# Kernel tuning notes

Measured on AMD Instinct MI355X. Metric: run time of the kernel, lower is better.

The kernel has to match this reference:

```python
import jax, jax.numpy as jnp
import numpy as np

BATCH, SEQ, CH, ORDER = 4, 8192, 512, 64


def setup_inputs() -> dict:
    key = jax.random.key(0)
    k1, k2, k3 = jax.random.split(key, 3)
    x = jax.random.normal(k1, (BATCH, SEQ, CH), dtype=jnp.float32)
    # RTF parameters: small init so the denominator polynomial 1 + sum a_i z^-i
    # stays well-conditioned (stable transfer function), as in the FSSM init.
    A = 0.01 * jax.random.normal(k2, (CH, ORDER), dtype=jnp.float32)
    B = 0.01 * jax.random.normal(k3, (CH, ORDER), dtype=jnp.float32)
    h0 = jnp.zeros((1,), dtype=jnp.float32)
    return {"x": x, "A": A, "B": B, "h0": h0}


def _rtf_kernel(A, B, L):
    # Evaluate H(z) = b(z)/a(z) at the L roots of unity, then irfft -> impulse response.
    C = A.shape[0]
    a = jnp.concatenate([jnp.ones((C, 1), A.dtype), A], axis=-1)  # (C, N+1), leading coeff 1
    a_f = jnp.fft.rfft(a, n=L, axis=-1)                           # (C, L//2+1)
    b_f = jnp.fft.rfft(B, n=L, axis=-1)
    return jnp.fft.irfft(b_f / a_f, n=L, axis=-1)                 # (C, L)


def reference(x, A, B, h0):
    Bt, L, C = x.shape
    K = _rtf_kernel(A, B, L)                                      # (C, L)
    n_fft = 2 * L                                                 # causal (linear) convolution
    x_f = jnp.fft.rfft(x, n=n_fft, axis=1)                        # (B, n_fft//2+1, C)
    k_f = jnp.fft.rfft(K, n=n_fft, axis=-1).T[None]               # (1, n_fft//2+1, C)
    h1 = jnp.fft.irfft(x_f * k_f, n=n_fft, axis=1)[:, :L]         # (B, L, C)
    y1 = h1 + h0 * x
    return jax.nn.gelu(y1)
```

## Files before the change

### kernel.cpp

```cpp
#include <hip/hip_runtime.h>
#include <stdint.h>

#define NBATCH 4
#define LSEQ   8192
#define CH     512
#define ORDER  64
#define KTAP   256
#define NW     9

typedef _Float16 half8 __attribute__((ext_vector_type(8)));
typedef __fp16   fp16x2 __attribute__((ext_vector_type(2)));
typedef float    f32x4 __attribute__((ext_vector_type(4)));

#define AFRAG_HALFS  ((size_t)CH * NW * 64 * 8)
#define WS_NEED      (AFRAG_HALFS * 2)

#define XROWB 1584
#define SMEMB (16 * XROWB)
#define PAIRS 392
#define TPB   4

__device__ __forceinline__ uint32_t pkrtz(float lo, float hi) {
    fp16x2 v = __builtin_amdgcn_cvt_pkrtz(lo, hi);
    return __builtin_bit_cast(uint32_t, v);
}

__global__ __launch_bounds__(256) void rtf_afrag(const float* __restrict__ A,
                                                 const float* __restrict__ B,
                                                 const float* __restrict__ h0,
                                                 _Float16* __restrict__ afr) {
    __shared__ float Ksh[4][KTAP];
    const int wv = threadIdx.x >> 6, lane = threadIdx.x & 63;
    const int c  = blockIdx.x * 4 + wv;
    const float a  = A[c * ORDER + lane];
    const float bc = B[c * ORDER + lane];
    const float h0v = h0[0];
    float s = 0.0f;
    for (int t = 0; t < KTAP; ++t) {
        const float s1 = __shfl(s, 0);
        const float bt = (t < ORDER) ? __shfl(bc, t) : 0.0f;
        const float y  = bt + s1;
        float su = __shfl_down(s, 1);
        if (lane == ORDER - 1) su = 0.0f;
        s = su - a * y;
        if (lane == 0) Ksh[wv][t] = (t == 0) ? (y + h0v) : y;
    }
    __syncthreads();
    const int i = lane & 15, g = lane >> 4;
    for (int w = 0; w < NW; ++w) {
        half8 hv;
#pragma unroll
        for (int e = 0; e < 8; ++e) {
            const int t = 32 * w + 15 + i - 8 * g - e;
            hv[e] = (_Float16)((t >= 0 && t < KTAP) ? Ksh[wv][t] : 0.0f);
        }
        *reinterpret_cast<half8*>(afr + ((size_t)(c * NW + w) * 64 + lane) * 8) = hv;
    }
}

__global__ __launch_bounds__(256, 2) void fir_pipe(const float* __restrict__ x,
                                                   const _Float16* __restrict__ afr,
                                                   float* __restrict__ out) {
    __shared__ __align__(16) char  xs[SMEMB];
    __shared__ float lout[16][260];
    const int gid     = blockIdx.x;
    const int logical = (gid & 7) * 64 + (gid >> 3);
    const int chgrp   = logical >> 4;
    const int bb      = (logical >> 2) & 3;
    const int qt      = logical & 3;
    const int nbase   = qt * (TPB * 512);
    const int c0      = chgrp * 16;

    const int q  = threadIdx.x & 3;
    const int pr = threadIdx.x >> 2;
    const float* xsrc = x + (size_t)bb * LSEQ * CH + c0 + q * 4;

    f32x4 L0[7], L1[7];

#define LOAD_TILE(N0K)                                                        \
    {                                                                         \
        _Pragma("unroll")                                                     \
        for (int i = 0; i < 7; ++i) {                                         \
            const int p = pr + 64 * i;                                        \
            f32x4 z = {0.f, 0.f, 0.f, 0.f};                                   \
            L0[i] = z; L1[i] = z;                                             \
            if (p < PAIRS) {                                                  \
                const int r0 = (N0K) - 271 + 2 * p;                           \
                if ((unsigned)r0 < LSEQ)                                      \
                    L0[i] = *reinterpret_cast<const f32x4*>(xsrc + (size_t)r0 * CH); \
                if ((unsigned)(r0 + 1) < LSEQ)                                \
                    L1[i] = *reinterpret_cast<const f32x4*>(xsrc + (size_t)(r0 + 1) * CH); \
            }                                                                 \
        }                                                                     \
    }

#define WRITE_XS()                                                            \
    {                                                                         \
        _Pragma("unroll")                                                     \
        for (int i = 0; i < 7; ++i) {                                         \
            const int p = pr + 64 * i;                                        \
            if (p < PAIRS) {                                                  \
                char* wb = xs + (size_t)(4 * q) * XROWB + 4 * p;              \
                *reinterpret_cast<uint32_t*>(wb + 0 * XROWB) = pkrtz(L0[i][0], L1[i][0]); \
                *reinterpret_cast<uint32_t*>(wb + 1 * XROWB) = pkrtz(L0[i][1], L1[i][1]); \
                *reinterpret_cast<uint32_t*>(wb + 2 * XROWB) = pkrtz(L0[i][2], L1[i][2]); \
                *reinterpret_cast<uint32_t*>(wb + 3 * XROWB) = pkrtz(L0[i][3], L1[i][3]); \
            }                                                                 \
        }                                                                     \
    }

    LOAD_TILE(nbase);
    WRITE_XS();
    LOAD_TILE(nbase + 512);
    __syncthreads();

    const int wid = threadIdx.x >> 6, lane = threadIdx.x & 63;
    const int j = lane & 15, g = lane >> 4;
    const int c0w = c0 + wid * 4;
    const _Float16* af = afr + (size_t)lane * 8;
    const int cq  = threadIdx.x & 3;
    const int nr0 = threadIdx.x >> 2;

#pragma unroll 1
    for (int k = 0; k < TPB; ++k) {
        const int n0 = nbase + 512 * k;

        f32x4 acc[2][4];
#pragma unroll
        for (int ti = 0; ti < 2; ++ti)
#pragma unroll
            for (int qq = 0; qq < 4; ++qq) acc[ti][qq] = (f32x4){0.f, 0.f, 0.f, 0.f};

        half8 a_cur[4], a_nxt[4];
#pragma unroll
        for (int qq = 0; qq < 4; ++qq)
            a_cur[qq] = *reinterpret_cast<const half8*>(af + (size_t)((c0w + qq) * NW + 0) * 512);
#pragma unroll
        for (int w = 0; w < NW; ++w) {
            if (w < NW - 1) {
#pragma unroll
                for (int qq = 0; qq < 4; ++qq)
                    a_nxt[qq] = *reinterpret_cast<const half8*>(af + (size_t)((c0w + qq) * NW + (w + 1)) * 512);
            }
            const int idx0 = 16 * j + 8 * g - 32 * w + 256;
#pragma unroll
            for (int ti = 0; ti < 2; ++ti) {
#pragma unroll
                for (int qq = 0; qq < 4; ++qq) {
                    const half8 bv = *reinterpret_cast<const half8*>(
                        xs + (size_t)(wid * 4 + qq) * XROWB + 2 * (idx0 + 256 * ti));
                    acc[ti][qq] = __builtin_amdgcn_mfma_f32_16x16x32_f16(a_cur[qq], bv, acc[ti][qq], 0, 0, 0);
                }
            }
#pragma unroll
            for (int qq = 0; qq < 4; ++qq) a_cur[qq] = a_nxt[qq];
        }

#pragma unroll
        for (int ti = 0; ti < 2; ++ti) {
            __syncthreads();
#pragma unroll
            for (int qq = 0; qq < 4; ++qq) {
                f32x4 o;
#pragma unroll
                for (int r = 0; r < 4; ++r) {
                    const float y  = acc[ti][qq][r];
                    const float wv = fmaf(y * y, 0.14270963f, 1.5957691f);
                    const float e  = __expf(y * wv);
                    o[r] = y - y * __builtin_amdgcn_rcpf(e + 1.0f);
                }
                *reinterpret_cast<f32x4*>(&lout[wid * 4 + qq][16 * j + 4 * g]) = o;
            }
            __syncthreads();
            float* obp = out + ((size_t)bb * LSEQ + n0 + ti * 256) * CH + c0 + 4 * cq;
#pragma unroll
            for (int it = 0; it < 4; ++it) {
                const int n = nr0 + 64 * it;
                f32x4 o;
                o[0] = lout[4 * cq + 0][n];
                o[1] = lout[4 * cq + 1][n];
                o[2] = lout[4 * cq + 2][n];
                o[3] = lout[4 * cq + 3][n];
                *reinterpret_cast<f32x4*>(obp + (size_t)n * CH) = o;
            }
        }

        if (k < TPB - 1) {
            WRITE_XS();
            if (k < TPB - 2) LOAD_TILE(nbase + 512 * (k + 2));
            __syncthreads();
        }
    }
#undef LOAD_TILE
#undef WRITE_XS
}

#define RINGF 32
#define CPBF  256
__global__ __launch_bounds__(ORDER) void rtf_impulse_fb(const float* __restrict__ A,
                                                        const float* __restrict__ B,
                                                        const float* __restrict__ h0,
                                                        float* __restrict__ kt4) {
    const int c = blockIdx.x, lane = threadIdx.x;
    const float a = A[c * ORDER + lane], bc = B[c * ORDER + lane], h0v = h0[0];
    float s = 0.0f;
    for (int t = 0; t < KTAP; ++t) {
        const float s1 = __shfl(s, 0);
        const float bt = (t < ORDER) ? __shfl(bc, t) : 0.0f;
        const float y  = bt + s1;
        float su = __shfl_down(s, 1);
        if (lane == ORDER - 1) su = 0.0f;
        s = su - a * y;
        if (lane == 0) kt4[((size_t)(t >> 2) * CH + c) * 4 + (t & 3)] = (t == 0) ? (y + h0v) : y;
    }
}
__global__ __launch_bounds__(CPBF) void fir_gelu_fb(const float* __restrict__ x,
                                                    const float* __restrict__ kt4,
                                                    float* __restrict__ out) {
    const int h = blockIdx.x;
    const int logical = ((h & 7) << 8) | (h >> 3);
    const int tile = logical & 255, sl = logical >> 8;
    const int cb = sl & 1, b = sl >> 1;
    const int c = cb * CPBF + threadIdx.x;
    const int n0 = tile * RINGF;
    const float* xb = x + (size_t)b * LSEQ * CH + c;
    const float4* kt4v = (const float4*)kt4;
    float acc[RINGF]; float ring[RINGF]; float px[2][8]; float kbuf[2][8];
#pragma unroll
    for (int r = 0; r < RINGF; ++r) acc[r] = 0.0f;
#pragma unroll
    for (int i = 0; i < RINGF; ++i) ring[i] = xb[(size_t)(n0 + i) * CH];
    {
        const float4 ka = kt4v[(size_t)0 * CH + c];
        const float4 kb = kt4v[(size_t)1 * CH + c];
        kbuf[0][0] = ka.x; kbuf[0][1] = ka.y; kbuf[0][2] = ka.z; kbuf[0][3] = ka.w;
        kbuf[0][4] = kb.x; kbuf[0][5] = kb.y; kbuf[0][6] = kb.z; kbuf[0][7] = kb.w;
#pragma unroll
        for (int g2 = 0; g2 < 8; ++g2) {
            const int m = n0 - 1 - g2;
            px[0][g2] = (m >= 0) ? xb[(size_t)m * CH] : 0.0f;
        }
    }
    for (int tb = 0; tb < KTAP; tb += RINGF) {
#pragma unroll
        for (int qq = 0; qq < 4; ++qq) {
            const int cur = qq & 1, nxt = cur ^ 1;
            const int tn = tb + 8 * (qq + 1);
            if (tn < KTAP) {
                const float4 ka = kt4v[(size_t)(tn >> 2) * CH + c];
                const float4 kb = kt4v[(size_t)((tn >> 2) + 1) * CH + c];
                kbuf[nxt][0] = ka.x; kbuf[nxt][1] = ka.y; kbuf[nxt][2] = ka.z; kbuf[nxt][3] = ka.w;
                kbuf[nxt][4] = kb.x; kbuf[nxt][5] = kb.y; kbuf[nxt][6] = kb.z; kbuf[nxt][7] = kb.w;
#pragma unroll
                for (int g2 = 0; g2 < 8; ++g2) {
                    const int m = n0 - tn - 1 - g2;
                    px[nxt][g2] = (m >= 0) ? xb[(size_t)m * CH] : 0.0f;
                }
            }
#pragma unroll
            for (int g2 = 0; g2 < 8; ++g2) {
                const int tq = 8 * qq + g2;
                const float kv = kbuf[cur][g2];
#pragma unroll
                for (int r = 0; r < RINGF; ++r)
                    acc[r] = fmaf(kv, ring[(r - tq) & (RINGF - 1)], acc[r]);
                ring[(RINGF - 1 - tq) & (RINGF - 1)] = px[cur][g2];
            }
        }
    }
    float* ob = out + ((size_t)b * LSEQ + n0) * CH + c;
#pragma unroll
    for (int r = 0; r < RINGF; ++r) {
        const float y = acc[r];
        const float wv = fmaf(y * y, 0.14270963f, 1.5957691f);
        const float e = __expf(y * wv);
        ob[(size_t)r * CH] = y - y * __builtin_amdgcn_rcpf(e + 1.0f);
    }
}

extern "C" void kernel_launch(void* const* d_in, const int* in_sizes, int n_in,
                              void* d_out, int out_size, void* d_ws, size_t ws_size,
                              hipStream_t stream) {
    const float* x  = (const float*)d_in[0];
    const float* A  = (const float*)d_in[1];
    const float* B  = (const float*)d_in[2];
    const float* h0 = (const float*)d_in[3];
    float* out = (float*)d_out;

    if (ws_size >= WS_NEED) {
        _Float16* afr = (_Float16*)d_ws;
        rtf_afrag<<<dim3(CH / 4), dim3(256), 0, stream>>>(A, B, h0, afr);
        fir_pipe<<<dim3(512), dim3(256), 0, stream>>>(x, afr, out);
    } else {
        float* kt4 = (float*)d_ws;
        rtf_impulse_fb<<<dim3(CH), dim3(ORDER), 0, stream>>>(A, B, h0, kt4);
        fir_gelu_fb<<<dim3((LSEQ / RINGF) * (CH / CPBF) * NBATCH), dim3(CPBF), 0, stream>>>(x, kt4, out);
    }
}
```

Before: 71.86 us.

## Split FIR kernel into producer and consumer warps with double-buffered LDS

Replaces the single-role 256-thread FIR kernel with a 512-thread kernel. Four warps stage the next x tile into a second LDS buffer while the other four run the MFMA convolution and GELU on the current tile, and all 512 threads share the output stores. The goal is to overlap global loads and fp16 packing with tensor-core work instead of interleaving them in one warp's register stream. In exchange, LDS per block roughly doubles, the block gets more barriers, and half the warps do no MFMA work, which may limit occupancy and change how many blocks fit per CU.

```diff
diff --git a/kernel.cpp b/kernel.cpp
--- a/kernel.cpp
+++ b/kernel.cpp
@@ -58,10 +58,10 @@
     }
 }
 
-__global__ __launch_bounds__(256, 2) void fir_pipe(const float* __restrict__ x,
-                                                   const _Float16* __restrict__ afr,
-                                                   float* __restrict__ out) {
-    __shared__ __align__(16) char  xs[SMEMB];
+__global__ __launch_bounds__(512, 4) void fir_pc(const float* __restrict__ x,
+                                                 const _Float16* __restrict__ afr,
+                                                 float* __restrict__ out) {
+    __shared__ __align__(16) char  xs2[2 * SMEMB];
     __shared__ float lout[16][260];
     const int gid     = blockIdx.x;
     const int logical = (gid & 7) * 64 + (gid >> 3);
@@ -71,14 +71,16 @@
     const int nbase   = qt * (TPB * 512);
     const int c0      = chgrp * 16;
 
+    const int wid      = threadIdx.x >> 6;
+    const bool producer = (wid < 4);
+
     const int q  = threadIdx.x & 3;
-    const int pr = threadIdx.x >> 2;
+    const int pr = (threadIdx.x & 255) >> 2;
     const float* xsrc = x + (size_t)bb * LSEQ * CH + c0 + q * 4;
 
-    f32x4 L0[7], L1[7];
-
-#define LOAD_TILE(N0K)                                                        \
+#define STAGE(N0K, BUF)                                                       \
     {                                                                         \
+        f32x4 L0[7], L1[7];                                                   \
         _Pragma("unroll")                                                     \
         for (int i = 0; i < 7; ++i) {                                         \
             const int p = pr + 64 * i;                                        \
@@ -92,15 +94,11 @@
                     L1[i] = *reinterpret_cast<const f32x4*>(xsrc + (size_t)(r0 + 1) * CH); \
             }                                                                 \
         }                                                                     \
-    }
-
-#define WRITE_XS()                                                            \
-    {                                                                         \
         _Pragma("unroll")                                                     \
         for (int i = 0; i < 7; ++i) {                                         \
             const int p = pr + 64 * i;                                        \
             if (p < PAIRS) {                                                  \
-                char* wb = xs + (size_t)(4 * q) * XROWB + 4 * p;              \
+                char* wb = (BUF) + (size_t)(4 * q) * XROWB + 4 * p;           \
                 *reinterpret_cast<uint32_t*>(wb + 0 * XROWB) = pkrtz(L0[i][0], L1[i][0]); \
                 *reinterpret_cast<uint32_t*>(wb + 1 * XROWB) = pkrtz(L0[i][1], L1[i][1]); \
                 *reinterpret_cast<uint32_t*>(wb + 2 * XROWB) = pkrtz(L0[i][2], L1[i][2]); \
@@ -109,90 +107,119 @@
         }                                                                     \
     }
 
-    LOAD_TILE(nbase);
-    WRITE_XS();
-    LOAD_TILE(nbase + 512);
+    const int cid  = threadIdx.x & 255;
+    const int cw   = cid >> 6;
+    const int lane = cid & 63;
+    const int j = lane & 15, g = lane >> 4;
+    const int c0w = c0 + cw * 4;
+    const _Float16* af = afr + (size_t)lane * 8;
+
+    const int scq = threadIdx.x & 3;
+    const int snr = threadIdx.x >> 2;
+
+    if (producer) STAGE(nbase, xs2);
     __syncthreads();
-
-    const int wid = threadIdx.x >> 6, lane = threadIdx.x & 63;
-    const int j = lane & 15, g = lane >> 4;
-    const int c0w = c0 + wid * 4;
-    const _Float16* af = afr + (size_t)lane * 8;
-    const int cq  = threadIdx.x & 3;
-    const int nr0 = threadIdx.x >> 2;
 
 #pragma unroll 1
     for (int k = 0; k < TPB; ++k) {
         const int n0 = nbase + 512 * k;
+        char* bufc = xs2 + (size_t)(k & 1) * SMEMB;
+        char* bufn = xs2 + (size_t)((k + 1) & 1) * SMEMB;
 
         f32x4 acc[2][4];
-#pragma unroll
-        for (int ti = 0; ti < 2; ++ti)
-#pragma unroll
-            for (int qq = 0; qq < 4; ++qq) acc[ti][qq] = (f32x4){0.f, 0.f, 0.f, 0.f};
-
-        half8 a_cur[4], a_nxt[4];
-#pragma unroll
-        for (int qq = 0; qq < 4; ++qq)
-            a_cur[qq] = *reinterpret_cast<const half8*>(af + (size_t)((c0w + qq) * NW + 0) * 512);
-#pragma unroll
-        for (int w = 0; w < NW; ++w) {
-            if (w < NW - 1) {
-#pragma unroll
-                for (int qq = 0; qq < 4; ++qq)
-                    a_nxt[qq] = *reinterpret_cast<const half8*>(af + (size_t)((c0w + qq) * NW + (w + 1)) * 512);
-            }
-            const int idx0 = 16 * j + 8 * g - 32 * w + 256;
-#pragma unroll
-            for (int ti = 0; ti < 2; ++ti) {
-#pragma unroll
-                for (int qq = 0; qq < 4; ++qq) {
-                    const half8 bv = *reinterpret_cast<const half8*>(
-                        xs + (size_t)(wid * 4 + qq) * XROWB + 2 * (idx0 + 256 * ti));
-                    acc[ti][qq] = __builtin_amdgcn_mfma_f32_16x16x32_f16(a_cur[qq], bv, acc[ti][qq], 0, 0, 0);
-                }
-            }
-#pragma unroll
-            for (int qq = 0; qq < 4; ++qq) a_cur[qq] = a_nxt[qq];
-        }
-
-#pragma unroll
-        for (int ti = 0; ti < 2; ++ti) {
-            __syncthreads();
+        if (producer) {
+            if (k < TPB - 1) STAGE(n0 + 512, bufn);
+        } else {
+#pragma unroll
+            for (int ti = 0; ti < 2; ++ti)
+#pragma unroll
+                for (int qq = 0; qq < 4; ++qq) acc[ti][qq] = (f32x4){0.f, 0.f, 0.f, 0.f};
+            half8 a_cur[4], a_nxt[4];
+#pragma unroll
+            for (int qq = 0; qq < 4; ++qq)
+                a_cur[qq] = *reinterpret_cast<const half8*>(af + (size_t)((c0w + qq) * NW + 0) * 512);
+#pragma unroll
+            for (int w = 0; w < NW; ++w) {
+                if (w < NW - 1) {
+#pragma unroll
+                    for (int qq = 0; qq < 4; ++qq)
+                        a_nxt[qq] = *reinterpret_cast<const half8*>(af + (size_t)((c0w + qq) * NW + (w + 1)) * 512);
+                }
+                const int idx0 = 16 * j + 8 * g - 32 * w + 256;
+#pragma unroll
+                for (int ti = 0; ti < 2; ++ti) {
+#pragma unroll
+                    for (int qq = 0; qq < 4; ++qq) {
+                        const half8 bv = *reinterpret_cast<const half8*>(
+                            bufc + (size_t)(cw * 4 + qq) * XROWB + 2 * (idx0 + 256 * ti));
+                        acc[ti][qq] = __builtin_amdgcn_mfma_f32_16x16x32_f16(a_cur[qq], bv, acc[ti][qq], 0, 0, 0);
+                    }
+                }
+#pragma unroll
+                for (int qq = 0; qq < 4; ++qq) a_cur[qq] = a_nxt[qq];
+            }
 #pragma unroll
             for (int qq = 0; qq < 4; ++qq) {
                 f32x4 o;
 #pragma unroll
                 for (int r = 0; r < 4; ++r) {
-                    const float y  = acc[ti][qq][r];
+                    const float y  = acc[0][qq][r];
                     const float wv = fmaf(y * y, 0.14270963f, 1.5957691f);
                     const float e  = __expf(y * wv);
                     o[r] = y - y * __builtin_amdgcn_rcpf(e + 1.0f);
                 }
-                *reinterpret_cast<f32x4*>(&lout[wid * 4 + qq][16 * j + 4 * g]) = o;
-            }
-            __syncthreads();
-            float* obp = out + ((size_t)bb * LSEQ + n0 + ti * 256) * CH + c0 + 4 * cq;
-#pragma unroll
-            for (int it = 0; it < 4; ++it) {
-                const int n = nr0 + 64 * it;
+                *reinterpret_cast<f32x4*>(&lout[cw * 4 + qq][16 * j + 4 * g]) = o;
+            }
+        }
+        __syncthreads();
+
+        {
+            float* obp = out + ((size_t)bb * LSEQ + n0) * CH + c0 + 4 * scq;
+#pragma unroll
+            for (int it = 0; it < 2; ++it) {
+                const int n = snr + 128 * it;
                 f32x4 o;
-                o[0] = lout[4 * cq + 0][n];
-                o[1] = lout[4 * cq + 1][n];
-                o[2] = lout[4 * cq + 2][n];
-                o[3] = lout[4 * cq + 3][n];
+                o[0] = lout[4 * scq + 0][n];
+                o[1] = lout[4 * scq + 1][n];
+                o[2] = lout[4 * scq + 2][n];
+                o[3] = lout[4 * scq + 3][n];
                 *reinterpret_cast<f32x4*>(obp + (size_t)n * CH) = o;
             }
         }
-
-        if (k < TPB - 1) {
-            WRITE_XS();
-            if (k < TPB - 2) LOAD_TILE(nbase + 512 * (k + 2));
-            __syncthreads();
-        }
-    }
-#undef LOAD_TILE
-#undef WRITE_XS
+        __syncthreads();
+
+        if (!producer) {
+#pragma unroll
+            for (int qq = 0; qq < 4; ++qq) {
+                f32x4 o;
+#pragma unroll
+                for (int r = 0; r < 4; ++r) {
+                    const float y  = acc[1][qq][r];
+                    const float wv = fmaf(y * y, 0.14270963f, 1.5957691f);
+                    const float e  = __expf(y * wv);
+                    o[r] = y - y * __builtin_amdgcn_rcpf(e + 1.0f);
+                }
+                *reinterpret_cast<f32x4*>(&lout[cw * 4 + qq][16 * j + 4 * g]) = o;
+            }
+        }
+        __syncthreads();
+
+        {
+            float* obp = out + ((size_t)bb * LSEQ + n0 + 256) * CH + c0 + 4 * scq;
+#pragma unroll
+            for (int it = 0; it < 2; ++it) {
+                const int n = snr + 128 * it;
+                f32x4 o;
+                o[0] = lout[4 * scq + 0][n];
+                o[1] = lout[4 * scq + 1][n];
+                o[2] = lout[4 * scq + 2][n];
+                o[3] = lout[4 * scq + 3][n];
+                *reinterpret_cast<f32x4*>(obp + (size_t)n * CH) = o;
+            }
+        }
+        __syncthreads();
+    }
+#undef STAGE
 }
 
 #define RINGF 32
@@ -290,7 +317,7 @@
     if (ws_size >= WS_NEED) {
         _Float16* afr = (_Float16*)d_ws;
         rtf_afrag<<<dim3(CH / 4), dim3(256), 0, stream>>>(A, B, h0, afr);
-        fir_pipe<<<dim3(512), dim3(256), 0, stream>>>(x, afr, out);
+        fir_pc<<<dim3(512), dim3(512), 0, stream>>>(x, afr, out);
     } else {
         float* kt4 = (float*)d_ws;
         rtf_impulse_fb<<<dim3(CH), dim3(ORDER), 0, stream>>>(A, B, h0, kt4);
```

Measured after the change: 103.8 us. +44.5%, slower.
